# Optimization experiments

Measured on AMD Instinct MI355X. Metric: run time of the kernel, lower is better.

The kernel has to match this reference:

```python
import jax, jax.numpy as jnp
import numpy as np

H = 2048          # hidden size
NH = 32           # query heads
NKV = 8           # kv heads
HD = H // NH      # head dim = 64
GROUPS = NH // NKV
S = 2048          # seq len
B = 1
SCALE = HD ** -0.5


def _rope_tables(seq, dim, base=10000.0):
    inv = 1.0 / (base ** (np.arange(0, dim, 2, dtype=np.float32) / dim))
    t = np.arange(seq, dtype=np.float32)
    freqs = np.outer(t, inv)                     # [S, dim/2]
    emb = np.concatenate([freqs, freqs], axis=-1)  # [S, dim]
    return jnp.asarray(np.cos(emb)), jnp.asarray(np.sin(emb))


def setup_inputs() -> dict:
    key = jax.random.key(0)
    ks = jax.random.split(key, 5)
    x = jax.random.normal(ks[0], (B, S, H), dtype=jnp.float32)
    wq = jax.random.normal(ks[1], (H, NH * HD), dtype=jnp.float32) * (H ** -0.5)
    wk = jax.random.normal(ks[2], (H, NKV * HD), dtype=jnp.float32) * (H ** -0.5)
    wv = jax.random.normal(ks[3], (H, NKV * HD), dtype=jnp.float32) * (H ** -0.5)
    wo = jax.random.normal(ks[4], (NH * HD, H), dtype=jnp.float32) * (H ** -0.5)
    cos, sin = _rope_tables(S, HD)
    mask = jnp.tril(jnp.ones((S, S), dtype=bool))[None, None]  # causal [1,1,S,S]
    return {"x": x, "wq": wq, "wk": wk, "wv": wv, "wo": wo,
            "cos": cos, "sin": sin, "mask": mask}


def _rotate_half(t):
    t1, t2 = jnp.split(t, 2, axis=-1)
    return jnp.concatenate([-t2, t1], axis=-1)


def reference(x, wq, wk, wv, wo, cos, sin, mask):
    b, s, _ = x.shape
    # projections
    q = (x @ wq).reshape(b, s, NH, HD).transpose(0, 2, 1, 3)    # [B,NH,S,HD]
    k = (x @ wk).reshape(b, s, NKV, HD).transpose(0, 2, 1, 3)   # [B,NKV,S,HD]
    v = (x @ wv).reshape(b, s, NKV, HD).transpose(0, 2, 1, 3)
    # RoPE (cos/sin broadcast over batch and heads)
    c = cos[None, None]; sn = sin[None, None]
    q = q * c + _rotate_half(q) * sn
    k = k * c + _rotate_half(k) * sn
    # GQA: repeat kv heads to match query heads
    k = jnp.repeat(k, GROUPS, axis=1)                           # [B,NH,S,HD]
    v = jnp.repeat(v, GROUPS, axis=1)
    # scores + causal mask + softmax (dropout p=0 -> identity in eval)
    scores = SCALE * jnp.einsum('bhqd,bhkd->bhqk', q, k)
    scores = jnp.where(mask, scores, -jnp.inf)
    attn = jax.nn.softmax(scores, axis=-1)
    out = jnp.einsum('bhqk,bhkd->bhqd', attn, v)
    out = out.transpose(0, 2, 1, 3).reshape(b, s, NH * HD)
    return out @ wo
```

## Files before the change

### kernel.cpp

```cpp
#include <hip/hip_runtime.h>

typedef unsigned short u16;
typedef unsigned u32;
typedef u16 u16x8 __attribute__((ext_vector_type(8)));
typedef u16 u16x4 __attribute__((ext_vector_type(4)));
typedef u32 u32x4 __attribute__((ext_vector_type(4)));
typedef __bf16 bf8 __attribute__((ext_vector_type(8)));
typedef float f32x4 __attribute__((ext_vector_type(4)));
typedef float f32x16 __attribute__((ext_vector_type(16)));

__device__ __forceinline__ u16 f2b(float f) {
  unsigned u = __float_as_uint(f);
  u += 0x7FFFu + ((u >> 16) & 1u);
  return (u16)(u >> 16);
}
__device__ __forceinline__ float b2f(u16 h) {
  return __uint_as_float(((unsigned)h) << 16);
}
__device__ __forceinline__ bf8 asbf8(u16x8 v) {
  return __builtin_bit_cast(bf8, v);
}
__device__ __forceinline__ void gll16(const u16* g, u16* l) {
  __builtin_amdgcn_global_load_lds(
      (const __attribute__((address_space(1))) unsigned*)(g),
      (__attribute__((address_space(3))) unsigned*)(l), 16, 0, 0);
}
__device__ __forceinline__ u32 cvtpk(float lo, float hi) {
  u32 r;
  asm("v_cvt_pk_bf16_f32 %0, %1, %2" : "=v"(r) : "v"(lo), "v"(hi));
  return r;
}
__device__ __forceinline__ void plswap(u32& a, u32& b) {
  asm("v_permlane32_swap_b32 %0, %1" : "+v"(a), "+v"(b));
}
__device__ __forceinline__ float ex2(float x) {
  return __builtin_amdgcn_exp2f(x);
}
#define MFMA32(A,B,C) __builtin_amdgcn_mfma_f32_32x32x16_bf16(A,B,C,0,0,0)


__global__ __launch_bounds__(256) void prep_all(const float* __restrict__ x,
                                                const float* __restrict__ wqp,
                                                const float* __restrict__ wkp,
                                                const float* __restrict__ wvp,
                                                const float* __restrict__ wop,
                                                u16* __restrict__ xb,
                                                u16* __restrict__ wqkvT,
                                                u16* __restrict__ woT) {
  const int bid = blockIdx.x;
  if (bid < 4096) {
    int i = (bid * 256 + threadIdx.x) * 4;
    float4 v = *(const float4*)(x + i);
    u16x4 o;
    o[0] = f2b(v.x); o[1] = f2b(v.y); o[2] = f2b(v.z); o[3] = f2b(v.w);
    *(u16x4*)(xb + i) = o;
    return;
  }
  __shared__ float tile[32][33];
  const float* in; u16* out; int N, bx, by;
  if (bid < 8192)       { int b = bid - 4096;  in = wqp; out = wqkvT;                         N = 2048; bx = b & 63; by = b >> 6; }
  else if (bid < 9216)  { int b = bid - 8192;  in = wkp; out = wqkvT + (size_t)2048 * 2048;   N = 512;  bx = b & 15; by = b >> 4; }
  else if (bid < 10240) { int b = bid - 9216;  in = wvp; out = wqkvT + (size_t)2560 * 2048;   N = 512;  bx = b & 15; by = b >> 4; }
  else                  { int b = bid - 10240; in = wop; out = woT;                           N = 2048; bx = b & 63; by = b >> 6; }
  const int K = 2048;
  int tx = threadIdx.x & 31, ty = threadIdx.x >> 5;
  int n0 = bx * 32, k0 = by * 32;
#pragma unroll
  for (int yy = 0; yy < 32; yy += 8)
    tile[ty + yy][tx] = in[(size_t)(k0 + ty + yy) * N + n0 + tx];
  __syncthreads();
#pragma unroll
  for (int yy = 0; yy < 32; yy += 8)
    out[(size_t)(n0 + ty + yy) * K + k0 + tx] = f2b(tile[tx][ty + yy]);
}

__global__ __launch_bounds__(256) void reduce_qkv(u16* __restrict__ p0,
                                                  const u16* __restrict__ p1,
                                                  u16* __restrict__ Kf,
                                                  u16* __restrict__ Vf,
                                                  const float* __restrict__ cs,
                                                  const float* __restrict__ sn) {
  int idx = blockIdx.x * 256 + threadIdx.x;
  int s = idx / 384, c8 = (idx % 384) * 8;
  size_t base = (size_t)s * 3072 + c8;
  if (c8 < 2560) {
    int hc = c8 & 63;
    if (hc >= 32) return;
    u16x8 a0 = *(const u16x8*)(p0 + base);
    u16x8 a1 = *(const u16x8*)(p1 + base);
    u16x8 b0 = *(const u16x8*)(p0 + base + 32);
    u16x8 b1 = *(const u16x8*)(p1 + base + 32);
    u16x8 oa, ob;
#pragma unroll
    for (int e = 0; e < 8; ++e) {
      float va = b2f(a0[e]) + b2f(a1[e]);
      float vb = b2f(b0[e]) + b2f(b1[e]);
      float c1 = cs[s * 64 + hc + e],      s1 = sn[s * 64 + hc + e];
      float c2 = cs[s * 64 + hc + 32 + e], s2 = sn[s * 64 + hc + 32 + e];
      oa[e] = f2b(va * c1 - vb * s1);
      ob[e] = f2b(vb * c2 + va * s2);
    }
    if (c8 < 2048) {
      *(u16x8*)(p0 + base)      = oa;
      *(u16x8*)(p0 + base + 32) = ob;
    } else {
      int kh = (c8 - 2048) >> 6;
      int d0 = hc;
      int b = s >> 5, la = s & 31;
      int j0 = d0 >> 4, hi0 = (d0 >> 3) & 1;
      size_t f0 = ((((size_t)(kh * 64 + b) * 4 + j0) * 2 + hi0) * 32 + la) * 8;
      size_t f1 = ((((size_t)(kh * 64 + b) * 4 + j0 + 2) * 2 + hi0) * 32 + la) * 8;
      *(u16x8*)(Kf + f0) = oa;
      *(u16x8*)(Kf + f1) = ob;
    }
  } else {
    u16x8 a0 = *(const u16x8*)(p0 + base);
    u16x8 a1 = *(const u16x8*)(p1 + base);
    int c = c8 - 2560;
    int kh = c >> 6, d0 = c & 63;
    int m = d0 >> 5, la0 = d0 & 31;
    int b = s >> 5, s5 = s & 31;
    int jj = s5 >> 4, hi = (s5 >> 3) & 1, e = s5 & 7;
    u16* dst = Vf + (((size_t)(kh * 64 + b) * 4 + m * 2 + jj) * 64 + hi * 32 + la0) * 8 + e;
#pragma unroll
    for (int i = 0; i < 8; ++i)
      dst[i * 8] = f2b(b2f(a0[i]) + b2f(a1[i]));
  }
}

__global__ __launch_bounds__(256) void reduce_out(const u16* __restrict__ p0,
                                                  const u16* __restrict__ p1,
                                                  float* __restrict__ out) {
  int idx = blockIdx.x * 256 + threadIdx.x;
  size_t base = (size_t)idx * 8;
  u16x8 a0 = *(const u16x8*)(p0 + base);
  u16x8 a1 = *(const u16x8*)(p1 + base);
  float4 lo, hi;
  lo.x = b2f(a0[0]) + b2f(a1[0]); lo.y = b2f(a0[1]) + b2f(a1[1]);
  lo.z = b2f(a0[2]) + b2f(a1[2]); lo.w = b2f(a0[3]) + b2f(a1[3]);
  hi.x = b2f(a0[4]) + b2f(a1[4]); hi.y = b2f(a0[5]) + b2f(a1[5]);
  hi.z = b2f(a0[6]) + b2f(a1[6]); hi.w = b2f(a0[7]) + b2f(a1[7]);
  *(float4*)(out + base)     = lo;
  *(float4*)(out + base + 4) = hi;
}


__global__ __launch_bounds__(256) void gemm_sk(const u16* __restrict__ A,
                                               const u16* __restrict__ Bt,
                                               u16* __restrict__ C0,
                                               u16* __restrict__ C1,
                                               int N, int Kfull, int KH) {
  __shared__ __align__(16) u16 As[128 * 64];
  __shared__ __align__(16) u16 Bs[128 * 64];
  const int t = threadIdx.x;
  const int lane = t & 63, wid = t >> 6;
  const int wm = (wid >> 1) * 64, wn = (wid & 1) * 64;
  const int la = lane & 15, lg = lane >> 4;
  const int m0 = blockIdx.y * 128, n0 = blockIdx.x * 128;
  const int kbeg = blockIdx.z * KH;
  u16* C = blockIdx.z ? C1 : C0;

  const int srow0 = wid * 32 + (lane >> 3);
  const int scolsw = (((lane & 7) ^ (lane >> 3))) * 8;
  const u16* Ap = A + (size_t)(m0 + srow0) * Kfull + kbeg + scolsw;
  const u16* Bp = Bt + (size_t)(n0 + srow0) * Kfull + kbeg + scolsw;
  u16* Adst = &As[wid * 2048];
  u16* Bdst = &Bs[wid * 2048];
  const size_t rstep8 = (size_t)8 * Kfull;

  f32x4 acc[4][4] = {};

  for (int k0 = 0; k0 < KH; k0 += 64) {
    __syncthreads();
#pragma unroll
    for (int cc = 0; cc < 4; ++cc)
      gll16(Ap + k0 + cc * rstep8, Adst + cc * 512);
#pragma unroll
    for (int cc = 0; cc < 4; ++cc)
      gll16(Bp + k0 + cc * rstep8, Bdst + cc * 512);
    __syncthreads();
#pragma unroll
    for (int kk = 0; kk < 2; ++kk) {
      bf8 af[4], bfr[4];
#pragma unroll
      for (int i = 0; i < 4; ++i) {
        const int row = wm + i * 16 + la;
        const int c8 = (kk * 4 + lg) ^ (row & 7);
        af[i] = asbf8(*(const u16x8*)(&As[row * 64 + c8 * 8]));
      }
#pragma unroll
      for (int j = 0; j < 4; ++j) {
        const int row = wn + j * 16 + la;
        const int c8 = (kk * 4 + lg) ^ (row & 7);
        bfr[j] = asbf8(*(const u16x8*)(&Bs[row * 64 + c8 * 8]));
      }
      __builtin_amdgcn_s_setprio(1);
#pragma unroll
      for (int i = 0; i < 4; ++i)
#pragma unroll
        for (int j = 0; j < 4; ++j)
          acc[i][j] = __builtin_amdgcn_mfma_f32_16x16x32_bf16(af[i], bfr[j],
                                                              acc[i][j], 0, 0, 0);
      __builtin_amdgcn_s_setprio(0);
    }
  }

#pragma unroll
  for (int i = 0; i < 4; ++i)
#pragma unroll
    for (int j = 0; j < 4; ++j)
#pragma unroll
      for (int r = 0; r < 4; ++r) {
        int row = m0 + wm + i * 16 + lg * 4 + r;
        int col = n0 + wn + j * 16 + la;
        C[(size_t)row * N + col] = f2b(acc[i][j][r]);
      }
}


#define STEPL(buf, bb) do {                                          \
    const u16* p_ = &smem[(((h2) << 1) | (buf)) * 4096 + lane8];     \
    bf8 K0 = asbf8(*(const u16x8*)(p_));                             \
    bf8 K1 = asbf8(*(const u16x8*)(p_ + 512));                       \
    bf8 K2 = asbf8(*(const u16x8*)(p_ + 1024));                      \
    bf8 K3 = asbf8(*(const u16x8*)(p_ + 1536));                      \
    bf8 V0 = asbf8(*(const u16x8*)(p_ + 2048));                      \
    bf8 V1 = asbf8(*(const u16x8*)(p_ + 2560));                      \
    bf8 V2 = asbf8(*(const u16x8*)(p_ + 3072));                      \
    bf8 V3 = asbf8(*(const u16x8*)(p_ + 3584));                      \
    f32x16 s = {};                                                   \
    __builtin_amdgcn_s_setprio(1);                                   \
    s = MFMA32(K0, qf0, s);                                          \
    s = MFMA32(K1, qf1, s);                                          \
    s = MFMA32(K2, qf2, s);                                          \
    s = MFMA32(K3, qf3, s);                                          \
    __builtin_amdgcn_s_setprio(0);                                   \
    if ((bb) == kmax) {                                              \
      _Pragma("unroll") for (int r = 0; r < 16; ++r) {               \
        int kvr = (bb) * 32 + (r & 3) + 8 * (r >> 2) + 4 * hi;       \
        if (kvr > q0w + la) s[r] = -1e30f;                           \
      }                                                              \
    }                                                                \
    _Pragma("unroll") for (int r = 0; r < 16; ++r)                   \
      s[r] = ex2(s[r] - 32.0f);                                      \
    float z0 = s[0] + s[1],   z1 = s[2] + s[3];                      \
    float z2 = s[4] + s[5],   z3 = s[6] + s[7];                      \
    float z4 = s[8] + s[9],   z5 = s[10] + s[11];                    \
    float z6 = s[12] + s[13], z7 = s[14] + s[15];                    \
    l_run += ((z0 + z1) + (z2 + z3)) + ((z4 + z5) + (z6 + z7));      \
    u32 c0 = cvtpk(s[0], s[1]),   c1 = cvtpk(s[2], s[3]);            \
    u32 c2 = cvtpk(s[4], s[5]),   c3 = cvtpk(s[6], s[7]);            \
    u32 c4 = cvtpk(s[8], s[9]),   c5 = cvtpk(s[10], s[11]);          \
    u32 c6 = cvtpk(s[12], s[13]), c7 = cvtpk(s[14], s[15]);          \
    plswap(c0, c2); plswap(c1, c3); plswap(c4, c6); plswap(c5, c7);  \
    u32x4 t0; t0[0] = c0; t0[1] = c1; t0[2] = c2; t0[3] = c3;        \
    u32x4 t1; t1[0] = c4; t1[1] = c5; t1[2] = c6; t1[3] = c7;        \
    bf8 pa0 = __builtin_bit_cast(bf8, t0);                           \
    bf8 pa1 = __builtin_bit_cast(bf8, t1);                           \
    __builtin_amdgcn_s_setprio(1);                                   \
    o0 = MFMA32(pa0, V0, o0);                                        \
    o0 = MFMA32(pa1, V1, o0);                                        \
    o1 = MFMA32(pa0, V2, o1);                                        \
    o1 = MFMA32(pa1, V3, o1);                                        \
    __builtin_amdgcn_s_setprio(0);                                   \
  } while (0)

#define STG(bb, buf) do {                                            \
    u16* d_ = &smem[((((h2) << 1) | (buf)) * 4096) + wq * 1024];     \
    const u16* kp_ = Kg + (size_t)(bb) * 2048 + wq * 1024 + lane8;   \
    const u16* vp_ = Vg + (size_t)(bb) * 2048 + wq * 1024 + lane8;   \
    gll16(kp_, d_);                                                  \
    gll16(kp_ + 512, d_ + 512);                                      \
    gll16(vp_, d_ + 2048);                                           \
    gll16(vp_ + 512, d_ + 2560);                                     \
  } while (0)

__global__ __launch_bounds__(256, 4) void attn_fwd(const u16* __restrict__ qkv,
                                                   const u16* __restrict__ Kf,
                                                   const u16* __restrict__ Vf,
                                                   u16* __restrict__ aout) {
  const int head = blockIdx.x;
  const int qt = 31 - (int)blockIdx.y;
  const int Q0 = qt * 64;
  const int Kb = qt * 2;
  const int nb = Kb + 2;
  const int ha = nb >> 1;
  const int kh = head >> 2;
  const int t = threadIdx.x;
  const int w = t >> 6, lane = t & 63;
  const int h2 = w >> 1;
  const int wq = w & 1;
  const int la = lane & 31;
  const int hi = lane >> 5;
  const int lane8 = lane * 8;
  const int q0w = Q0 + 32 * wq;
  const int kmax = Kb + wq;

  __shared__ __align__(16) u16 smem[16384];
  __shared__ float lM[4][32];

  bf8 qf0, qf1, qf2, qf3;
  {
    const u16* qp = qkv + (size_t)(q0w + la) * 3072 + head * 64 + hi * 8;
    const float SC = 0.125f * 1.44269504088896340736f;
#define QLOAD(dst, kk) do {                                          \
      u16x8 v = *(const u16x8*)(qp + (kk) * 16);                     \
      u16x8 sv;                                                      \
      _Pragma("unroll") for (int e = 0; e < 8; ++e)                  \
        sv[e] = f2b(b2f(v[e]) * SC);                                 \
      dst = asbf8(sv);                                               \
    } while (0)
    QLOAD(qf0, 0); QLOAD(qf1, 1); QLOAD(qf2, 2); QLOAD(qf3, 3);
#undef QLOAD
  }

  const u16* Kg = Kf + (size_t)kh * 131072;
  const u16* Vg = Vf + (size_t)kh * 131072;

  f32x16 o0 = {}, o1 = {};
  float l_run = 0.f;

  STG(h2 ? ha : 0, 0);

  for (int i = 0; i < ha; ++i) {
    const bool pf = (i + 1 < ha);
    if (pf) STG(h2 ? (ha + i + 1) : (i + 1), (i + 1) & 1);
    if (pf) asm volatile("s_waitcnt vmcnt(4)" ::: "memory");
    else    asm volatile("s_waitcnt vmcnt(0)" ::: "memory");
    __builtin_amdgcn_s_barrier();
    __builtin_amdgcn_sched_barrier(0);
    const int bb = h2 ? (ha + i) : i;
    if (bb <= kmax) STEPL(i & 1, bb);
    __builtin_amdgcn_sched_barrier(0);
    __builtin_amdgcn_s_barrier();
  }

  {
    float lt = l_run + __shfl_xor(l_run, 32);
    if (lane < 32) lM[w][lane] = lt;
#pragma unroll
    for (int r = 0; r < 16; ++r) {
      int crow = (r & 3) + 8 * (r >> 2) + 4 * hi;
      smem[(w * 32 + crow) * 72 + la]      = f2b(o0[r]);
      smem[(w * 32 + crow) * 72 + la + 32] = f2b(o1[r]);
    }
  }
  __syncthreads();

#pragma unroll
  for (int it = 0; it < 2; ++it) {
    const int id = t + it * 256;
    const int q = id >> 3, d0 = (id & 7) * 8;
    const int wA = q >> 5, crow = q & 31;
    float inv = 1.0f / (lM[wA][crow] + lM[wA + 2][crow]);
    u16x8 a = *(const u16x8*)&smem[((wA)     * 32 + crow) * 72 + d0];
    u16x8 b = *(const u16x8*)&smem[((wA + 2) * 32 + crow) * 72 + d0];
    u16x8 outv;
#pragma unroll
    for (int j = 0; j < 8; ++j)
      outv[j] = f2b((b2f(a[j]) + b2f(b[j])) * inv);
    *(u16x8*)(aout + (size_t)(Q0 + q) * 2048 + head * 64 + d0) = outv;
  }
}


extern "C" void kernel_launch(void* const* d_in, const int* in_sizes, int n_in,
                              void* d_out, int out_size, void* d_ws, size_t ws_size,
                              hipStream_t stream) {
  (void)in_sizes; (void)n_in; (void)out_size; (void)ws_size;
  const float* x  = (const float*)d_in[0];
  const float* wq = (const float*)d_in[1];
  const float* wk = (const float*)d_in[2];
  const float* wv = (const float*)d_in[3];
  const float* wo = (const float*)d_in[4];
  const float* cs = (const float*)d_in[5];
  const float* sn = (const float*)d_in[6];

  u16* ws    = (u16*)d_ws;
  u16* xb    = ws;
  u16* wqkvT = ws + 4194304;
  u16* qkv   = ws + 10485760;
  u16* woT   = ws + 16777216;
  u16* ext   = ws + 20971520;
  u16* Kf    = wqkvT;
  u16* Vf    = wqkvT + 1048576;
  u16* aout  = xb;
  u16* op0   = qkv;
  u16* op1   = ext;

  prep_all<<<14336, 256, 0, stream>>>(x, wq, wk, wv, wo, xb, wqkvT, woT);

  gemm_sk<<<dim3(24, 16, 2), 256, 0, stream>>>(xb, wqkvT, qkv, ext, 3072, 2048, 1024);
  reduce_qkv<<<3072, 256, 0, stream>>>(qkv, ext, Kf, Vf, cs, sn);
  attn_fwd<<<dim3(32, 32), 256, 0, stream>>>(qkv, Kf, Vf, aout);
  gemm_sk<<<dim3(16, 16, 2), 256, 0, stream>>>(aout, woT, op0, op1, 2048, 2048, 1024);
  reduce_out<<<2048, 256, 0, stream>>>(op0, op1, (float*)d_out);
}
```

Before: 130.4 us.

## Pair causal query tiles per block and triple-buffer K/V staging in attention

```diff
diff --git a/kernel.cpp b/kernel.cpp
--- a/kernel.cpp
+++ b/kernel.cpp
@@ -219,7 +219,7 @@
 
 
 #define STEPL(buf, bb) do {                                          \
-    const u16* p_ = &smem[(((h2) << 1) | (buf)) * 4096 + lane8];     \
+    const u16* p_ = &smem[(h2 * 3 + (buf)) * 4096 + lane8];          \
     bf8 K0 = asbf8(*(const u16x8*)(p_));                             \
     bf8 K1 = asbf8(*(const u16x8*)(p_ + 512));                       \
     bf8 K2 = asbf8(*(const u16x8*)(p_ + 1024));                      \
@@ -242,7 +242,7 @@
       }                                                              \
     }                                                                \
     _Pragma("unroll") for (int r = 0; r < 16; ++r)                   \
-      s[r] = ex2(s[r] - 32.0f);                                      \
+      s[r] = ex2(s[r]);                                              \
     float z0 = s[0] + s[1],   z1 = s[2] + s[3];                      \
     float z2 = s[4] + s[5],   z3 = s[6] + s[7];                      \
     float z4 = s[8] + s[9],   z5 = s[10] + s[11];                    \
@@ -266,7 +266,7 @@
   } while (0)
 
 #define STG(bb, buf) do {                                            \
-    u16* d_ = &smem[((((h2) << 1) | (buf)) * 4096) + wq * 1024];     \
+    u16* d_ = &smem[((h2 * 3 + (buf)) * 4096) + wq * 1024];          \
     const u16* kp_ = Kg + (size_t)(bb) * 2048 + wq * 1024 + lane8;   \
     const u16* vp_ = Vg + (size_t)(bb) * 2048 + wq * 1024 + lane8;   \
     gll16(kp_, d_);                                                  \
@@ -280,11 +280,7 @@
                                                    const u16* __restrict__ Vf,
                                                    u16* __restrict__ aout) {
   const int head = blockIdx.x;
-  const int qt = 31 - (int)blockIdx.y;
-  const int Q0 = qt * 64;
-  const int Kb = qt * 2;
-  const int nb = Kb + 2;
-  const int ha = nb >> 1;
+  const int pid  = blockIdx.y;
   const int kh = head >> 2;
   const int t = threadIdx.x;
   const int w = t >> 6, lane = t & 63;
@@ -293,73 +289,89 @@
   const int la = lane & 31;
   const int hi = lane >> 5;
   const int lane8 = lane * 8;
-  const int q0w = Q0 + 32 * wq;
-  const int kmax = Kb + wq;
-
-  __shared__ __align__(16) u16 smem[16384];
+
+  __shared__ __align__(16) u16 smem[24576];
   __shared__ float lM[4][32];
-
-  bf8 qf0, qf1, qf2, qf3;
-  {
-    const u16* qp = qkv + (size_t)(q0w + la) * 3072 + head * 64 + hi * 8;
-    const float SC = 0.125f * 1.44269504088896340736f;
-#define QLOAD(dst, kk) do {                                          \
-      u16x8 v = *(const u16x8*)(qp + (kk) * 16);                     \
-      u16x8 sv;                                                      \
-      _Pragma("unroll") for (int e = 0; e < 8; ++e)                  \
-        sv[e] = f2b(b2f(v[e]) * SC);                                 \
-      dst = asbf8(sv);                                               \
-    } while (0)
-    QLOAD(qf0, 0); QLOAD(qf1, 1); QLOAD(qf2, 2); QLOAD(qf3, 3);
-#undef QLOAD
-  }
 
   const u16* Kg = Kf + (size_t)kh * 131072;
   const u16* Vg = Vf + (size_t)kh * 131072;
 
-  f32x16 o0 = {}, o1 = {};
-  float l_run = 0.f;
-
-  STG(h2 ? ha : 0, 0);
-
-  for (int i = 0; i < ha; ++i) {
-    const bool pf = (i + 1 < ha);
-    if (pf) STG(h2 ? (ha + i + 1) : (i + 1), (i + 1) & 1);
-    if (pf) asm volatile("s_waitcnt vmcnt(4)" ::: "memory");
-    else    asm volatile("s_waitcnt vmcnt(0)" ::: "memory");
-    __builtin_amdgcn_s_barrier();
-    __builtin_amdgcn_sched_barrier(0);
-    const int bb = h2 ? (ha + i) : i;
-    if (bb <= kmax) STEPL(i & 1, bb);
-    __builtin_amdgcn_sched_barrier(0);
-    __builtin_amdgcn_s_barrier();
-  }
-
-  {
-    float lt = l_run + __shfl_xor(l_run, 32);
-    if (lane < 32) lM[w][lane] = lt;
-#pragma unroll
-    for (int r = 0; r < 16; ++r) {
-      int crow = (r & 3) + 8 * (r >> 2) + 4 * hi;
-      smem[(w * 32 + crow) * 72 + la]      = f2b(o0[r]);
-      smem[(w * 32 + crow) * 72 + la + 32] = f2b(o1[r]);
-    }
-  }
-  __syncthreads();
-
-#pragma unroll
-  for (int it = 0; it < 2; ++it) {
-    const int id = t + it * 256;
-    const int q = id >> 3, d0 = (id & 7) * 8;
-    const int wA = q >> 5, crow = q & 31;
-    float inv = 1.0f / (lM[wA][crow] + lM[wA + 2][crow]);
-    u16x8 a = *(const u16x8*)&smem[((wA)     * 32 + crow) * 72 + d0];
-    u16x8 b = *(const u16x8*)&smem[((wA + 2) * 32 + crow) * 72 + d0];
-    u16x8 outv;
-#pragma unroll
-    for (int j = 0; j < 8; ++j)
-      outv[j] = f2b((b2f(a[j]) + b2f(b[j])) * inv);
-    *(u16x8*)(aout + (size_t)(Q0 + q) * 2048 + head * 64 + d0) = outv;
+#pragma unroll 1
+  for (int pass = 0; pass < 2; ++pass) {
+    const int qt = pass ? (31 - pid) : pid;
+    const int Q0 = qt * 64;
+    const int Kb = qt * 2;
+    const int ha = Kb / 2 + 1;
+    const int q0w = Q0 + 32 * wq;
+    const int kmax = Kb + wq;
+    const int mybase = h2 ? ha : 0;
+
+    bf8 qf0, qf1, qf2, qf3;
+    {
+      const u16* qp = qkv + (size_t)(q0w + la) * 3072 + head * 64 + hi * 8;
+      const float SC = 0.125f * 1.44269504088896340736f;
+#define QLOAD(dst, kk) do {                                          \
+        u16x8 v = *(const u16x8*)(qp + (kk) * 16);                   \
+        u16x8 sv;                                                    \
+        _Pragma("unroll") for (int e = 0; e < 8; ++e)                \
+          sv[e] = f2b(b2f(v[e]) * SC);                               \
+        dst = asbf8(sv);                                             \
+      } while (0)
+      QLOAD(qf0, 0); QLOAD(qf1, 1); QLOAD(qf2, 2); QLOAD(qf3, 3);
+#undef QLOAD
+    }
+
+    f32x16 o0 = {}, o1 = {};
+    float l_run = 0.f;
+
+    STG(mybase, 0);
+
+    int buf = 0;
+    for (int i = 0; i < ha; ++i) {
+      const bool pf = (i + 1 < ha);
+      const int nbuf = (buf == 2) ? 0 : buf + 1;
+      if (pf) {
+        STG(mybase + i + 1, nbuf);
+        asm volatile("s_waitcnt vmcnt(4)" ::: "memory");
+      } else {
+        asm volatile("s_waitcnt vmcnt(0)" ::: "memory");
+      }
+      __builtin_amdgcn_s_barrier();
+      __builtin_amdgcn_sched_barrier(0);
+      const int bb = mybase + i;
+      if (bb <= kmax) STEPL(buf, bb);
+      __builtin_amdgcn_sched_barrier(0);
+      buf = nbuf;
+    }
+    __syncthreads();
+
+    {
+      float lt = l_run + __shfl_xor(l_run, 32);
+      if (lane < 32) lM[w][lane] = lt;
+#pragma unroll
+      for (int r = 0; r < 16; ++r) {
+        int crow = (r & 3) + 8 * (r >> 2) + 4 * hi;
+        smem[(w * 32 + crow) * 72 + la]      = f2b(o0[r]);
+        smem[(w * 32 + crow) * 72 + la + 32] = f2b(o1[r]);
+      }
+    }
+    __syncthreads();
+
+#pragma unroll
+    for (int it = 0; it < 2; ++it) {
+      const int id = t + it * 256;
+      const int q = id >> 3, d0 = (id & 7) * 8;
+      const int wA = q >> 5, crow = q & 31;
+      float inv = 1.0f / (lM[wA][crow] + lM[wA + 2][crow]);
+      u16x8 a = *(const u16x8*)&smem[((wA)     * 32 + crow) * 72 + d0];
+      u16x8 b = *(const u16x8*)&smem[((wA + 2) * 32 + crow) * 72 + d0];
+      u16x8 outv;
+#pragma unroll
+      for (int j = 0; j < 8; ++j)
+        outv[j] = f2b((b2f(a[j]) + b2f(b[j])) * inv);
+      *(u16x8*)(aout + (size_t)(Q0 + q) * 2048 + head * 64 + d0) = outv;
+    }
+    __syncthreads();
   }
 }
 
@@ -392,7 +404,7 @@
 
   gemm_sk<<<dim3(24, 16, 2), 256, 0, stream>>>(xb, wqkvT, qkv, ext, 3072, 2048, 1024);
   reduce_qkv<<<3072, 256, 0, stream>>>(qkv, ext, Kf, Vf, cs, sn);
-  attn_fwd<<<dim3(32, 32), 256, 0, stream>>>(qkv, Kf, Vf, aout);
+  attn_fwd<<<dim3(32, 16), 256, 0, stream>>>(qkv, Kf, Vf, aout);
   gemm_sk<<<dim3(16, 16, 2), 256, 0, stream>>>(aout, woT, op0, op1, 2048, 2048, 1024);
   reduce_out<<<2048, 256, 0, stream>>>(op0, op1, (float*)d_out);
 }
```

Result: no change. 131.7 us (+1.0%).

## Give each wave a private KV staging buffer and drop per-step block barriers

Applied to the files above, without the earlier changes.

```diff
diff --git a/kernel.cpp b/kernel.cpp
--- a/kernel.cpp
+++ b/kernel.cpp
@@ -218,61 +218,18 @@
 }
 
 
-#define STEPL(buf, bb) do {                                          \
-    const u16* p_ = &smem[(((h2) << 1) | (buf)) * 4096 + lane8];     \
-    bf8 K0 = asbf8(*(const u16x8*)(p_));                             \
-    bf8 K1 = asbf8(*(const u16x8*)(p_ + 512));                       \
-    bf8 K2 = asbf8(*(const u16x8*)(p_ + 1024));                      \
-    bf8 K3 = asbf8(*(const u16x8*)(p_ + 1536));                      \
-    bf8 V0 = asbf8(*(const u16x8*)(p_ + 2048));                      \
-    bf8 V1 = asbf8(*(const u16x8*)(p_ + 2560));                      \
-    bf8 V2 = asbf8(*(const u16x8*)(p_ + 3072));                      \
-    bf8 V3 = asbf8(*(const u16x8*)(p_ + 3584));                      \
-    f32x16 s = {};                                                   \
-    __builtin_amdgcn_s_setprio(1);                                   \
-    s = MFMA32(K0, qf0, s);                                          \
-    s = MFMA32(K1, qf1, s);                                          \
-    s = MFMA32(K2, qf2, s);                                          \
-    s = MFMA32(K3, qf3, s);                                          \
-    __builtin_amdgcn_s_setprio(0);                                   \
-    if ((bb) == kmax) {                                              \
-      _Pragma("unroll") for (int r = 0; r < 16; ++r) {               \
-        int kvr = (bb) * 32 + (r & 3) + 8 * (r >> 2) + 4 * hi;       \
-        if (kvr > q0w + la) s[r] = -1e30f;                           \
-      }                                                              \
-    }                                                                \
-    _Pragma("unroll") for (int r = 0; r < 16; ++r)                   \
-      s[r] = ex2(s[r] - 32.0f);                                      \
-    float z0 = s[0] + s[1],   z1 = s[2] + s[3];                      \
-    float z2 = s[4] + s[5],   z3 = s[6] + s[7];                      \
-    float z4 = s[8] + s[9],   z5 = s[10] + s[11];                    \
-    float z6 = s[12] + s[13], z7 = s[14] + s[15];                    \
-    l_run += ((z0 + z1) + (z2 + z3)) + ((z4 + z5) + (z6 + z7));      \
-    u32 c0 = cvtpk(s[0], s[1]),   c1 = cvtpk(s[2], s[3]);            \
-    u32 c2 = cvtpk(s[4], s[5]),   c3 = cvtpk(s[6], s[7]);            \
-    u32 c4 = cvtpk(s[8], s[9]),   c5 = cvtpk(s[10], s[11]);          \
-    u32 c6 = cvtpk(s[12], s[13]), c7 = cvtpk(s[14], s[15]);          \
-    plswap(c0, c2); plswap(c1, c3); plswap(c4, c6); plswap(c5, c7);  \
-    u32x4 t0; t0[0] = c0; t0[1] = c1; t0[2] = c2; t0[3] = c3;        \
-    u32x4 t1; t1[0] = c4; t1[1] = c5; t1[2] = c6; t1[3] = c7;        \
-    bf8 pa0 = __builtin_bit_cast(bf8, t0);                           \
-    bf8 pa1 = __builtin_bit_cast(bf8, t1);                           \
-    __builtin_amdgcn_s_setprio(1);                                   \
-    o0 = MFMA32(pa0, V0, o0);                                        \
-    o0 = MFMA32(pa1, V1, o0);                                        \
-    o1 = MFMA32(pa0, V2, o1);                                        \
-    o1 = MFMA32(pa1, V3, o1);                                        \
-    __builtin_amdgcn_s_setprio(0);                                   \
-  } while (0)
-
-#define STG(bb, buf) do {                                            \
-    u16* d_ = &smem[((((h2) << 1) | (buf)) * 4096) + wq * 1024];     \
-    const u16* kp_ = Kg + (size_t)(bb) * 2048 + wq * 1024 + lane8;   \
-    const u16* vp_ = Vg + (size_t)(bb) * 2048 + wq * 1024 + lane8;   \
+#define STG(bb) do {                                                 \
+    u16* d_ = &smem[w * 4096];                                       \
+    const u16* kp_ = Kg + (size_t)(bb) * 2048 + lane8;               \
+    const u16* vp_ = Vg + (size_t)(bb) * 2048 + lane8;               \
     gll16(kp_, d_);                                                  \
     gll16(kp_ + 512, d_ + 512);                                      \
+    gll16(kp_ + 1024, d_ + 1024);                                    \
+    gll16(kp_ + 1536, d_ + 1536);                                    \
     gll16(vp_, d_ + 2048);                                           \
     gll16(vp_ + 512, d_ + 2560);                                     \
+    gll16(vp_ + 1024, d_ + 3072);                                    \
+    gll16(vp_ + 1536, d_ + 3584);                                    \
   } while (0)
 
 __global__ __launch_bounds__(256, 4) void attn_fwd(const u16* __restrict__ qkv,
@@ -283,8 +240,7 @@
   const int qt = 31 - (int)blockIdx.y;
   const int Q0 = qt * 64;
   const int Kb = qt * 2;
-  const int nb = Kb + 2;
-  const int ha = nb >> 1;
+  const int ha = Kb / 2 + 1;
   const int kh = head >> 2;
   const int t = threadIdx.x;
   const int w = t >> 6, lane = t & 63;
@@ -295,6 +251,8 @@
   const int lane8 = lane * 8;
   const int q0w = Q0 + 32 * wq;
   const int kmax = Kb + wq;
+  const int mybase = h2 ? ha : 0;
+  const int myn = min(ha, kmax - mybase + 1);
 
   __shared__ __align__(16) u16 smem[16384];
   __shared__ float lM[4][32];
@@ -320,20 +278,65 @@
   f32x16 o0 = {}, o1 = {};
   float l_run = 0.f;
 
-  STG(h2 ? ha : 0, 0);
-
-  for (int i = 0; i < ha; ++i) {
-    const bool pf = (i + 1 < ha);
-    if (pf) STG(h2 ? (ha + i + 1) : (i + 1), (i + 1) & 1);
-    if (pf) asm volatile("s_waitcnt vmcnt(4)" ::: "memory");
-    else    asm volatile("s_waitcnt vmcnt(0)" ::: "memory");
-    __builtin_amdgcn_s_barrier();
+  if (myn > 0) STG(mybase);
+
+  for (int i = 0; i < myn; ++i) {
+    asm volatile("s_waitcnt vmcnt(0)" ::: "memory");
     __builtin_amdgcn_sched_barrier(0);
-    const int bb = h2 ? (ha + i) : i;
-    if (bb <= kmax) STEPL(i & 1, bb);
+    const int bb = mybase + i;
+    const u16* p_ = &smem[w * 4096 + lane8];
+    bf8 K0 = asbf8(*(const u16x8*)(p_));
+    bf8 K1 = asbf8(*(const u16x8*)(p_ + 512));
+    bf8 K2 = asbf8(*(const u16x8*)(p_ + 1024));
+    bf8 K3 = asbf8(*(const u16x8*)(p_ + 1536));
+    bf8 V0 = asbf8(*(const u16x8*)(p_ + 2048));
+    bf8 V1 = asbf8(*(const u16x8*)(p_ + 2560));
+    bf8 V2 = asbf8(*(const u16x8*)(p_ + 3072));
+    bf8 V3 = asbf8(*(const u16x8*)(p_ + 3584));
+    asm volatile("s_waitcnt lgkmcnt(0)" ::: "memory");
     __builtin_amdgcn_sched_barrier(0);
-    __builtin_amdgcn_s_barrier();
-  }
+    if (i + 1 < myn) STG(bb + 1);
+    f32x16 s = {};
+    __builtin_amdgcn_s_setprio(1);
+    s = MFMA32(K0, qf0, s);
+    s = MFMA32(K1, qf1, s);
+    s = MFMA32(K2, qf2, s);
+    s = MFMA32(K3, qf3, s);
+    __builtin_amdgcn_s_setprio(0);
+    if (bb == kmax) {
+#pragma unroll
+      for (int r = 0; r < 16; ++r) {
+        int kvr = bb * 32 + (r & 3) + 8 * (r >> 2) + 4 * hi;
+        if (kvr > q0w + la) s[r] = -1e30f;
+      }
+    }
+#pragma unroll
+    for (int r = 0; r < 16; ++r) s[r] = ex2(s[r]);
+    {
+      float z0 = s[0] + s[1],   z1 = s[2] + s[3];
+      float z2 = s[4] + s[5],   z3 = s[6] + s[7];
+      float z4 = s[8] + s[9],   z5 = s[10] + s[11];
+      float z6 = s[12] + s[13], z7 = s[14] + s[15];
+      l_run += ((z0 + z1) + (z2 + z3)) + ((z4 + z5) + (z6 + z7));
+    }
+    u32 c0 = cvtpk(s[0], s[1]),   c1 = cvtpk(s[2], s[3]);
+    u32 c2 = cvtpk(s[4], s[5]),   c3 = cvtpk(s[6], s[7]);
+    u32 c4 = cvtpk(s[8], s[9]),   c5 = cvtpk(s[10], s[11]);
+    u32 c6 = cvtpk(s[12], s[13]), c7 = cvtpk(s[14], s[15]);
+    plswap(c0, c2); plswap(c1, c3); plswap(c4, c6); plswap(c5, c7);
+    u32x4 t0; t0[0] = c0; t0[1] = c1; t0[2] = c2; t0[3] = c3;
+    u32x4 t1; t1[0] = c4; t1[1] = c5; t1[2] = c6; t1[3] = c7;
+    bf8 pa0 = __builtin_bit_cast(bf8, t0);
+    bf8 pa1 = __builtin_bit_cast(bf8, t1);
+    __builtin_amdgcn_s_setprio(1);
+    o0 = MFMA32(pa0, V0, o0);
+    o0 = MFMA32(pa1, V1, o0);
+    o1 = MFMA32(pa0, V2, o1);
+    o1 = MFMA32(pa1, V3, o1);
+    __builtin_amdgcn_s_setprio(0);
+  }
+
+  __syncthreads();
 
   {
     float lt = l_run + __shfl_xor(l_run, 32);
```

Result: no change. 129.8 us (-0.5%).
